# Optimization experiments

Hardware: AMD Instinct MI355X
Metric: run time of the kernel (lower is better)

Reference implementation:

```python
import jax, jax.numpy as jnp
import numpy as np

N_NODES = 150000
N_EDGES = 2400000


def setup_inputs() -> dict:
    key = jax.random.key(0)
    ks = jax.random.split(key, 16)
    d_in, d_h = 6, 32

    def lin(k, fan_in, fan_out):
        # torch nn.Linear default init: U(-1/sqrt(fan_in), 1/sqrt(fan_in))
        bound = 1.0 / np.sqrt(fan_in)
        kw, kb = jax.random.split(k)
        W = jax.random.uniform(kw, (fan_in, fan_out), jnp.float32, -bound, bound)
        b = jax.random.uniform(kb, (fan_out,), jnp.float32, -bound, bound)
        return W, b

    x = jax.random.normal(ks[0], (N_NODES, d_in), jnp.float32)
    edge_index = jax.random.randint(ks[1], (2, N_EDGES), 0, N_NODES, jnp.int64 if jax.config.jax_enable_x64 else jnp.int32)
    W1, b1 = lin(ks[2], d_in, d_h)
    W2, b2 = lin(ks[3], d_h, d_h)
    Wt1, bt1 = lin(ks[4], d_h, d_h // 2)
    Wt2, bt2 = lin(ks[5], d_h // 2, 1)
    Wa1, ba1 = lin(ks[6], d_h, d_h // 2)
    Wa2, ba2 = lin(ks[7], d_h // 2, 6)
    return {"x": x, "edge_index": edge_index,
            "W1": W1, "b1": b1, "W2": W2, "b2": b2,
            "Wt1": Wt1, "bt1": bt1, "Wt2": Wt2, "bt2": bt2,
            "Wa1": Wa1, "ba1": ba1, "Wa2": Wa2, "ba2": ba2}


def gcn_conv(x, src, dst, W, b, n):
    """PyG GCNConv: D^{-1/2}(A+I)D^{-1/2} X W + b (self-loops added)."""
    xw = x @ W  # [N, out]
    ones = jnp.ones(src.shape[0], xw.dtype)
    deg = jax.ops.segment_sum(ones, dst, num_segments=n) + 1.0  # +1 for self-loop
    dinv = jax.lax.rsqrt(deg)
    norm = dinv[src] * dinv[dst]  # [E]
    agg = jax.ops.segment_sum(xw[src] * norm[:, None], dst, num_segments=n)
    agg = agg + xw * (dinv * dinv)[:, None]  # self-loop contribution
    return agg + b


def mlp_head(h, Wa, ba, Wb, bb):
    return jax.nn.relu(h @ Wa + ba) @ Wb + bb


def reference(x, edge_index, W1, b1, W2, b2, Wt1, bt1, Wt2, bt2, Wa1, ba1, Wa2, ba2):
    n = x.shape[0]
    src, dst = edge_index[0], edge_index[1]
    h = jax.nn.relu(gcn_conv(x, src, dst, W1, b1, n))
    features = gcn_conv(h, src, dst, W2, b2, n)
    topology_logits = mlp_head(features, Wt1, bt1, Wt2, bt2)  # [N, 1]
    attributes = mlp_head(features, Wa1, ba1, Wa2, ba2)       # [N, 6]
    normals = attributes[:, :3]
    uvs = attributes[:, 3:]
    return topology_logits, normals, uvs, features
```

## Files before the change

kernel.cpp:

```cpp
#include <hip/hip_runtime.h>
#include <hip/hip_bf16.h>

typedef __hip_bfloat16 bf16;

__device__ __forceinline__ float b2f(bf16 v) { return __bfloat162float(v); }
__device__ __forceinline__ bf16  f2b(float v){ return __float2bfloat16(v); }

__device__ __forceinline__ float loadF(const void* p, int i, int isf32) {
    return isf32 ? ((const float*)p)[i] : b2f(((const bf16*)p)[i]);
}
__device__ __forceinline__ int loadI(const void* p, long long i, int isi64) {
    return isi64 ? (int)((const long long*)p)[i] : ((const int*)p)[i];
}

#define NSBW 512
#define SBSH 9
#define CHUNK_A 4096
#define BCAP 12288

__global__ void sniff_kernel(const void* xv, const void* eiv, int* flags) {
    int lane = threadIdx.x;
    const bf16* xb = (const bf16*)xv;
    int big = 0;
#pragma unroll
    for (int k = 0; k < 4; k++) {
        float v = fabsf(b2f(xb[lane * 4 + k]));
        if (v > 1e6f) big = 1;
    }
    unsigned long long bigmask = __ballot(big);
    const int* e32 = (const int*)eiv;
    int nz = (lane < 32) ? (e32[2 * lane + 1] != 0) : 0;
    unsigned long long nzmask = __ballot(nz);
    if (lane == 0) {
        flags[0] = (__popcll(bigmask) >= 8) ? 1 : 0;
        flags[1] = (nzmask == 0ULL) ? 1 : 0;
    }
}

__global__ void zero_f32(float* __restrict__ p, long long cnt) {
    long long i = (long long)blockIdx.x * blockDim.x + threadIdx.x;
    if (i < cnt) p[i] = 0.f;
}
__global__ void zero_i32(int* __restrict__ p, long long cnt) {
    long long i = (long long)blockIdx.x * blockDim.x + threadIdx.x;
    if (i < cnt) p[i] = 0;
}

__global__ void sb_count(const void* ei, int* __restrict__ sbcnt, int E, int n,
                         const int* __restrict__ flags) {
    __shared__ int h[512];
    int tid = threadIdx.x;
    h[tid] = 0; h[tid + 256] = 0;
    __syncthreads();
    int idf = flags[1];
    long long bs = (long long)blockIdx.x * CHUNK_A;
#pragma unroll 4
    for (int it = 0; it < CHUNK_A / 256; it++) {
        long long e = bs + it * 256 + tid;
        if (e < E) {
            int s = loadI(ei, e, idf);
            int d = loadI(ei, (long long)E + e, idf);
            if ((unsigned)s < (unsigned)n && (unsigned)d < (unsigned)n)
                atomicAdd(&h[d >> SBSH], 1);
        }
    }
    __syncthreads();
    if (h[tid]) atomicAdd(&sbcnt[tid * 16], h[tid]);
    if (h[tid + 256]) atomicAdd(&sbcnt[(tid + 256) * 16], h[tid + 256]);
}

__global__ void sb_scan(const int* __restrict__ sbcnt, int* __restrict__ sboff,
                        int* __restrict__ sbcur, int NSB) {
    __shared__ int lds[512];
    int t = threadIdx.x;
    int v = (t < NSB) ? sbcnt[t * 16] : 0;
    lds[t] = v; __syncthreads();
    for (int off = 1; off < 512; off <<= 1) {
        int tv = (t >= off) ? lds[t - off] : 0;
        __syncthreads();
        lds[t] += tv;
        __syncthreads();
    }
    if (t < NSB) { int ex = lds[t] - v; sboff[t] = ex; sbcur[t * 16] = ex; }
    if (t == 0) sboff[NSB] = lds[511];
}

__global__ void sb_scatter(const void* ei, int* __restrict__ sbcur,
                           unsigned* __restrict__ tmp, int E, int n,
                           const int* __restrict__ flags) {
    __shared__ int h[512];
    __shared__ int base[512];
    int tid = threadIdx.x;
    h[tid] = 0; h[tid + 256] = 0;
    __syncthreads();
    int idf = flags[1];
    long long bs = (long long)blockIdx.x * CHUNK_A;
#pragma unroll 4
    for (int it = 0; it < CHUNK_A / 256; it++) {
        long long e = bs + it * 256 + tid;
        if (e < E) {
            int s = loadI(ei, e, idf);
            int d = loadI(ei, (long long)E + e, idf);
            if ((unsigned)s < (unsigned)n && (unsigned)d < (unsigned)n)
                atomicAdd(&h[d >> SBSH], 1);
        }
    }
    __syncthreads();
    int c0 = h[tid];       if (c0) base[tid] = atomicAdd(&sbcur[tid * 16], c0);
    int c1 = h[tid + 256]; if (c1) base[tid + 256] = atomicAdd(&sbcur[(tid + 256) * 16], c1);
    h[tid] = 0; h[tid + 256] = 0;
    __syncthreads();
#pragma unroll 4
    for (int it = 0; it < CHUNK_A / 256; it++) {
        long long e = bs + it * 256 + tid;
        if (e < E) {
            int s = loadI(ei, e, idf);
            int d = loadI(ei, (long long)E + e, idf);
            if ((unsigned)s < (unsigned)n && (unsigned)d < (unsigned)n) {
                int b = d >> SBSH;
                int r = atomicAdd(&h[b], 1);
                tmp[base[b] + r] = (unsigned)s | ((unsigned)(d & (NSBW - 1)) << 18);
            }
        }
    }
}

__global__ __launch_bounds__(512) void sb_sort(const unsigned* __restrict__ tmp,
                                               const int* __restrict__ sboff,
                                               int* __restrict__ rowptr, int* __restrict__ adj,
                                               int n, int NSB) {
    __shared__ unsigned buf[BCAP];
    __shared__ int deg[NSBW], sc[NSBW], excl[NSBW], cur[NSBW];
    int sb = blockIdx.x, tid = threadIdx.x;
    int beg = sboff[sb], end = sboff[sb + 1], len = end - beg;
    deg[tid] = 0; cur[tid] = 0;
    __syncthreads();
    bool fits = (len <= BCAP);
    for (int i = tid; i < len; i += 512) {
        unsigned p = tmp[beg + i];
        if (fits) buf[i] = p;
        atomicAdd(&deg[p >> 18], 1);
    }
    __syncthreads();
    sc[tid] = deg[tid]; __syncthreads();
    for (int off = 1; off < 512; off <<= 1) {
        int tv = (tid >= off) ? sc[tid - off] : 0;
        __syncthreads();
        sc[tid] += tv;
        __syncthreads();
    }
    excl[tid] = sc[tid] - deg[tid];
    int node = (sb << SBSH) + tid;
    if (node < n) rowptr[node] = beg + excl[tid];
    if (sb == 0 && tid == 0) rowptr[n] = sboff[NSB];
    __syncthreads();
    for (int i = tid; i < len; i += 512) {
        unsigned p = fits ? buf[i] : tmp[beg + i];
        int dl = (int)(p >> 18);
        int pos = excl[dl] + atomicAdd(&cur[dl], 1);
        adj[beg + pos] = (int)(p & 0x3FFFFu);
    }
}

__global__ void prep2_kernel(const int* __restrict__ rowptr, const void* xv,
                             float* __restrict__ dinv, float* __restrict__ z,
                             int n, const int* __restrict__ flags) {
    int i = blockIdx.x * blockDim.x + threadIdx.x;
    if (i >= n) return;
    int xf = flags[0];
    int deg = rowptr[i + 1] - rowptr[i];
    float dv = rsqrtf((float)deg + 1.0f);
    dinv[i] = dv;
    float* zr = z + (size_t)i * 8;
#pragma unroll
    for (int k = 0; k < 6; k++) zr[k] = loadF(xv, i * 6 + k, xf) * dv;
    zr[6] = dv; zr[7] = 0.f;
}

__global__ void gcn1_kernel(const int* __restrict__ rowptr, const int* __restrict__ adj,
                            const float* __restrict__ z,
                            const void* W1v, const void* b1v, const void* W2v,
                            bf16* __restrict__ Y2b, int n, const int* __restrict__ flags) {
    __shared__ float sW1[6 * 32];
    __shared__ float sW2[32 * 32];
    __shared__ float sb1[32];
    int xf = flags[0];
    int tid = threadIdx.x;
    if (tid < 192) sW1[tid] = loadF(W1v, tid, xf);
    for (int i = tid; i < 1024; i += blockDim.x) sW2[i] = loadF(W2v, i, xf);
    if (tid < 32) sb1[tid] = loadF(b1v, tid, xf);
    __syncthreads();
    long long t = (long long)blockIdx.x * blockDim.x + tid;
    int node = (int)(t >> 5), j = (int)(t & 31);
    if (node >= n) return;
    int base = rowptr[node], end = rowptr[node + 1];
    float a0 = 0.f, a1 = 0.f, a2 = 0.f, a3 = 0.f;
    int half4 = (j & 1) * 4;
    for (int i0 = base; i0 < end; i0 += 16) {
        int eidx = i0 + (j >> 1);
        if (eidx < end) {
            int s = adj[eidx];
            const float4 v = *(const float4*)(z + (size_t)s * 8 + half4);
            a0 += v.x; a1 += v.y; a2 += v.z; a3 += v.w;
        }
    }
#pragma unroll
    for (int off = 2; off <= 16; off <<= 1) {
        a0 += __shfl_xor(a0, off, 32); a1 += __shfl_xor(a1, off, 32);
        a2 += __shfl_xor(a2, off, 32); a3 += __shfl_xor(a3, off, 32);
    }
    float S0 = __shfl(a0, 0, 32), S1 = __shfl(a1, 0, 32), S2 = __shfl(a2, 0, 32);
    float S3 = __shfl(a3, 0, 32), S4 = __shfl(a0, 1, 32), S5 = __shfl(a1, 1, 32);
    const float* zs = z + (size_t)node * 8;
    float dv = zs[6];
    S0 += zs[0]; S1 += zs[1]; S2 += zs[2]; S3 += zs[3]; S4 += zs[4]; S5 += zs[5];
    float v = S0 * sW1[j];
    v = fmaf(S1, sW1[32 + j], v);
    v = fmaf(S2, sW1[64 + j], v);
    v = fmaf(S3, sW1[96 + j], v);
    v = fmaf(S4, sW1[128 + j], v);
    v = fmaf(S5, sW1[160 + j], v);
    float h = fmaxf(fmaf(dv, v, sb1[j]), 0.f);
    float y2 = 0.f;
#pragma unroll
    for (int kk = 0; kk < 32; kk++) y2 = fmaf(__shfl(h, kk, 32), sW2[kk * 32 + j], y2);
    Y2b[(size_t)node * 32 + j] = f2b(y2 * dv);
}

__global__ void gcn2_kernel(const int* __restrict__ rowptr, const int* __restrict__ adj,
                            const bf16* __restrict__ Y2b, const float* __restrict__ dinv,
                            const void* b2v,
                            const void* Wt1v, const void* bt1v, const void* Wt2v, const void* bt2v,
                            const void* Wa1v, const void* ba1v, const void* Wa2v, const void* ba2v,
                            float* __restrict__ out, int n, const int* __restrict__ flags) {
    __shared__ float sWt1[32 * 16], sWa1[32 * 16], sWt2[16], sWa2[16 * 6];
    __shared__ float sbt1[16], sba1[16], sba2[6], sb2[32];
    __shared__ float sbt2;
    int xf = flags[0];
    int tid = threadIdx.x;
    for (int i = tid; i < 32 * 16; i += blockDim.x) {
        sWt1[i] = loadF(Wt1v, i, xf);
        sWa1[i] = loadF(Wa1v, i, xf);
    }
    for (int i = tid; i < 16 * 6; i += blockDim.x) sWa2[i] = loadF(Wa2v, i, xf);
    if (tid < 16) { sWt2[tid] = loadF(Wt2v, tid, xf); sbt1[tid] = loadF(bt1v, tid, xf); sba1[tid] = loadF(ba1v, tid, xf); }
    if (tid < 32) sb2[tid] = loadF(b2v, tid, xf);
    if (tid < 6) sba2[tid] = loadF(ba2v, tid, xf);
    if (tid == 0) sbt2 = loadF(bt2v, 0, xf);
    __syncthreads();
    long long t = (long long)blockIdx.x * blockDim.x + tid;
    int node = (int)(t >> 5), j = (int)(t & 31);
    if (node >= n) return;
    int base = rowptr[node], end = rowptr[node + 1];
    float agg = 0.f;
    for (int i0 = base; i0 < end; i0 += 32) {
        int rem = end - i0;
        int sv = (j < rem) ? adj[i0 + j] : 0;
        int mm = (rem < 32) ? rem : 32;
        int kk = 0;
        for (; kk + 4 <= mm; kk += 4) {
            int s0 = __shfl(sv, kk, 32), s1 = __shfl(sv, kk + 1, 32);
            int s2 = __shfl(sv, kk + 2, 32), s3 = __shfl(sv, kk + 3, 32);
            float q0 = b2f(Y2b[(size_t)s0 * 32 + j]);
            float q1 = b2f(Y2b[(size_t)s1 * 32 + j]);
            float q2 = b2f(Y2b[(size_t)s2 * 32 + j]);
            float q3 = b2f(Y2b[(size_t)s3 * 32 + j]);
            agg += (q0 + q1) + (q2 + q3);
        }
        for (; kk < mm; kk++) {
            int s0 = __shfl(sv, kk, 32);
            agg += b2f(Y2b[(size_t)s0 * 32 + j]);
        }
    }
    float dv = dinv[node];
    float f = fmaf(dv, agg + b2f(Y2b[(size_t)node * 32 + j]), sb2[j]);
    __builtin_nontemporal_store(f, &out[(size_t)n * 7 + (size_t)node * 32 + j]);
    float acc = 0.f;
#pragma unroll
    for (int k = 0; k < 32; k++) {
        float fk = __shfl(f, k, 32);
        float w = (j < 16) ? sWt1[k * 16 + j] : sWa1[k * 16 + (j - 16)];
        acc = fmaf(fk, w, acc);
    }
    float u = fmaxf(acc + ((j < 16) ? sbt1[j] : sba1[j - 16]), 0.f);
    float o = 0.f;
#pragma unroll
    for (int k = 0; k < 16; k++) {
        float ut = __shfl(u, k, 32);
        float ua = __shfl(u, 16 + k, 32);
        float w = (j == 0) ? sWt2[k] : ((j < 7) ? sWa2[k * 6 + (j - 1)] : 0.f);
        o = fmaf((j == 0) ? ut : ua, w, o);
    }
    if (j == 0)      out[node] = o + sbt2;
    else if (j < 4)  out[(size_t)n     + (size_t)node * 3 + (j - 1)] = o + sba2[j - 1];
    else if (j < 7)  out[(size_t)n * 4 + (size_t)node * 3 + (j - 4)] = o + sba2[j - 1];
}

__global__ void count_kernel(const void* ei, float* __restrict__ deg, int E, int n,
                             const int* __restrict__ flags) {
    int e = blockIdx.x * blockDim.x + threadIdx.x;
    if (e >= E) return;
    int d = loadI(ei, (long long)E + e, flags[1]);
    if ((unsigned)d < (unsigned)n) atomicAdd(&deg[d], 1.0f);
}
__global__ void dinv_kernel(float* __restrict__ dinv, int n) {
    int i = blockIdx.x * blockDim.x + threadIdx.x;
    if (i < n) dinv[i] = rsqrtf(dinv[i] + 1.0f);
}
__global__ void scatter1_kernel(const void* ei, const void* xv, const void* W1v,
                                const float* __restrict__ dinv, float* __restrict__ A,
                                int E, int n, const int* __restrict__ flags) {
    __shared__ float sW1[6 * 32];
    int xf = flags[0], idf = flags[1];
    int tid = threadIdx.x;
    if (tid < 192) sW1[tid] = loadF(W1v, tid, xf);
    __syncthreads();
    long long t = (long long)blockIdx.x * blockDim.x + tid;
    int e = (int)(t >> 5), j = (int)(t & 31);
    if (e >= E) return;
    int s = loadI(ei, e, idf);
    int d = loadI(ei, (long long)E + e, idf);
    if ((unsigned)s >= (unsigned)n || (unsigned)d >= (unsigned)n) return;
    float dv = dinv[s];
    float y = 0.f;
#pragma unroll
    for (int k = 0; k < 6; k++) y = fmaf(loadF(xv, s * 6 + k, xf), sW1[k * 32 + j], y);
    atomicAdd(&A[(size_t)d * 32 + j], y * dv);
}
__global__ void fused_mid_kernel(const float* __restrict__ A, const void* xv,
                                 const float* __restrict__ dinv,
                                 const void* W1v, const void* b1v, const void* W2v,
                                 float* __restrict__ Yf, int n, const int* __restrict__ flags) {
    __shared__ float sW1[6 * 32];
    __shared__ float sW2[32 * 32];
    __shared__ float sb1[32];
    int xf = flags[0];
    int tid = threadIdx.x;
    if (tid < 192) sW1[tid] = loadF(W1v, tid, xf);
    for (int i = tid; i < 32 * 32; i += blockDim.x) sW2[i] = loadF(W2v, i, xf);
    if (tid < 32) sb1[tid] = loadF(b1v, tid, xf);
    __syncthreads();
    long long t = (long long)blockIdx.x * blockDim.x + tid;
    int node = (int)(t >> 5), j = (int)(t & 31);
    if (node >= n) return;
    float dv = dinv[node];
    float xw = 0.f;
#pragma unroll
    for (int k = 0; k < 6; k++) xw = fmaf(loadF(xv, node * 6 + k, xf), sW1[k * 32 + j], xw);
    float h = fmaxf(dv * A[t] + dv * dv * xw + sb1[j], 0.f);
    float y2 = 0.f;
#pragma unroll
    for (int k = 0; k < 32; k++) y2 = fmaf(__shfl(h, k, 32), sW2[k * 32 + j], y2);
    Yf[t] = y2 * dv;
}
__global__ void scatter2_kernel(const void* ei, const float* __restrict__ Yf,
                                float* __restrict__ A, int E, int n,
                                const int* __restrict__ flags) {
    int idf = flags[1];
    long long t = (long long)blockIdx.x * blockDim.x + threadIdx.x;
    int e = (int)(t >> 5), j = (int)(t & 31);
    if (e >= E) return;
    int s = loadI(ei, e, idf);
    int d = loadI(ei, (long long)E + e, idf);
    if ((unsigned)s >= (unsigned)n || (unsigned)d >= (unsigned)n) return;
    atomicAdd(&A[(size_t)d * 32 + j], Yf[(size_t)s * 32 + j]);
}
__global__ void out_kernel(const float* __restrict__ A, const float* __restrict__ dinv,
                           const void* b2v,
                           const void* Wt1v, const void* bt1v, const void* Wt2v, const void* bt2v,
                           const void* Wa1v, const void* ba1v, const void* Wa2v, const void* ba2v,
                           float* __restrict__ out, int n, const int* __restrict__ flags) {
    __shared__ float sWt1[32 * 16], sWa1[32 * 16], sWt2[16], sWa2[16 * 6];
    __shared__ float sbt1[16], sba1[16], sba2[6], sb2[32];
    __shared__ float sbt2;
    int xf = flags[0];
    int tid = threadIdx.x;
    for (int i = tid; i < 32 * 16; i += blockDim.x) { sWt1[i] = loadF(Wt1v, i, xf); sWa1[i] = loadF(Wa1v, i, xf); }
    for (int i = tid; i < 16 * 6; i += blockDim.x) sWa2[i] = loadF(Wa2v, i, xf);
    if (tid < 16) { sWt2[tid] = loadF(Wt2v, tid, xf); sbt1[tid] = loadF(bt1v, tid, xf); sba1[tid] = loadF(ba1v, tid, xf); }
    if (tid < 32) sb2[tid] = loadF(b2v, tid, xf);
    if (tid < 6) sba2[tid] = loadF(ba2v, tid, xf);
    if (tid == 0) sbt2 = loadF(bt2v, 0, xf);
    __syncthreads();
    long long t = (long long)blockIdx.x * blockDim.x + tid;
    int node = (int)(t >> 5), j = (int)(t & 31);
    if (node >= n) return;
    float* Yf = out + (size_t)n * 7;
    float dv = dinv[node];
    float f = dv * (A[t] + Yf[t]) + sb2[j];
    Yf[t] = f;
    float acc = 0.f;
#pragma unroll
    for (int k = 0; k < 32; k++) {
        float fk = __shfl(f, k, 32);
        float w = (j < 16) ? sWt1[k * 16 + j] : sWa1[k * 16 + (j - 16)];
        acc = fmaf(fk, w, acc);
    }
    float u = fmaxf(acc + ((j < 16) ? sbt1[j] : sba1[j - 16]), 0.f);
    float o = 0.f;
#pragma unroll
    for (int k = 0; k < 16; k++) {
        float ut = __shfl(u, k, 32);
        float ua = __shfl(u, 16 + k, 32);
        float w = (j == 0) ? sWt2[k] : ((j < 7) ? sWa2[k * 6 + (j - 1)] : 0.f);
        o = fmaf((j == 0) ? ut : ua, w, o);
    }
    if (j == 0)      out[node] = o + sbt2;
    else if (j < 4)  out[(size_t)n     + (size_t)node * 3 + (j - 1)] = o + sba2[j - 1];
    else if (j < 7)  out[(size_t)n * 4 + (size_t)node * 3 + (j - 4)] = o + sba2[j - 1];
}

extern "C" void kernel_launch(void* const* d_in, const int* in_sizes, int n_in,
                              void* d_out, int out_size, void* d_ws, size_t ws_size,
                              hipStream_t stream) {
    const void* x   = d_in[0];
    const void* ei  = d_in[1];
    const void* W1  = d_in[2];
    const void* b1  = d_in[3];
    const void* W2  = d_in[4];
    const void* b2  = d_in[5];
    const void* Wt1 = d_in[6];
    const void* bt1 = d_in[7];
    const void* Wt2 = d_in[8];
    const void* bt2 = d_in[9];
    const void* Wa1 = d_in[10];
    const void* ba1 = d_in[11];
    const void* Wa2 = d_in[12];
    const void* ba2 = d_in[13];

    int n = in_sizes[0] / 6;
    int E = in_sizes[1] / 2;

    const int B = 256;
    float* out = (float*)d_out;
    char* ws = (char*)d_ws;

    int NSB = (n + NSBW - 1) >> SBSH;
    size_t nw  = (size_t)((n + 63) & ~63);
    size_t Ew  = (size_t)((E + 63) & ~63);
    size_t Mw  = (16 * nw > Ew) ? 16 * nw : Ew;
    size_t w_sbc = 0;
    size_t w_sbo = 8192;
    size_t w_scu = 8192 + 576;
    size_t w_flg = w_scu + 8192;
    size_t w_row = w_flg + 64;
    size_t w_div = w_row + nw + 64;
    size_t w_z   = w_div + nw;
    size_t w_un  = w_z + 8 * nw;
    size_t w_adj = w_un + Mw;
    size_t need  = (w_adj + Ew) * 4;

    if (ws_size >= need && n <= (1 << 18)) {
        int*      sbcnt = (int*)(ws + w_sbc * 4);
        int*      sboff = (int*)(ws + w_sbo * 4);
        int*      sbcur = (int*)(ws + w_scu * 4);
        int*      flags = (int*)(ws + w_flg * 4);
        int*      rowptr= (int*)(ws + w_row * 4);
        float*    dinv  = (float*)(ws + w_div * 4);
        float*    z     = (float*)(ws + w_z * 4);
        unsigned* tmp   = (unsigned*)(ws + w_un * 4);
        bf16*     Y2b   = (bf16*)(ws + w_un * 4);
        int*      adj   = (int*)(ws + w_adj * 4);

        int grid_a = (int)(((long long)E + CHUNK_A - 1) / CHUNK_A);
        int grid_nodes32 = (int)(((long long)n * 32 + B - 1) / B);

        sniff_kernel<<<1, 64, 0, stream>>>(x, ei, flags);
        zero_i32<<<(8192 * 2 + 576 + B - 1) / B, B, 0, stream>>>(sbcnt, 8192 * 2 + 576);
        sb_count<<<grid_a, B, 0, stream>>>(ei, sbcnt, E, n, flags);
        sb_scan<<<1, 512, 0, stream>>>(sbcnt, sboff, sbcur, NSB);
        sb_scatter<<<grid_a, B, 0, stream>>>(ei, sbcur, tmp, E, n, flags);
        sb_sort<<<NSB, 512, 0, stream>>>(tmp, sboff, rowptr, adj, n, NSB);
        prep2_kernel<<<(n + B - 1) / B, B, 0, stream>>>(rowptr, x, dinv, z, n, flags);
        gcn1_kernel<<<grid_nodes32, B, 0, stream>>>(rowptr, adj, z, W1, b1, W2, Y2b, n, flags);
        gcn2_kernel<<<grid_nodes32, B, 0, stream>>>(rowptr, adj, Y2b, dinv, b2,
                                                    Wt1, bt1, Wt2, bt2, Wa1, ba1, Wa2, ba2,
                                                    out, n, flags);
        return;
    }

    size_t n_pad = (size_t)((n + 63) & ~63);
    float* A     = (float*)ws;
    float* dinvF = (float*)(ws + (size_t)32 * n * 4);
    int* flagsF  = (int*)(ws + ((size_t)32 * n + n_pad) * 4);
    float* Yf    = out + (size_t)n * 7;

    long long zcnt = (long long)32 * n + (long long)n_pad;
    int grid_zero  = (int)((zcnt + B - 1) / B);
    int grid_zeroA = (int)(((long long)32 * n + B - 1) / B);
    int grid_nodes = (int)(((long long)n * 32 + B - 1) / B);
    int grid_edges = (int)(((long long)E * 32 + B - 1) / B);

    sniff_kernel<<<1, 64, 0, stream>>>(x, ei, flagsF);
    zero_f32<<<grid_zero, B, 0, stream>>>(A, zcnt);
    count_kernel<<<(E + B - 1) / B, B, 0, stream>>>(ei, dinvF, E, n, flagsF);
    dinv_kernel<<<(n + B - 1) / B, B, 0, stream>>>(dinvF, n);
    scatter1_kernel<<<grid_edges, B, 0, stream>>>(ei, x, W1, dinvF, A, E, n, flagsF);
    fused_mid_kernel<<<grid_nodes, B, 0, stream>>>(A, x, dinvF, W1, b1, W2, Yf, n, flagsF);
    zero_f32<<<grid_zeroA, B, 0, stream>>>(A, (long long)32 * n);
    scatter2_kernel<<<grid_edges, B, 0, stream>>>(ei, Yf, A, E, n, flagsF);
    out_kernel<<<grid_nodes, B, 0, stream>>>(A, dinvF, b2, Wt1, bt1, Wt2, bt2,
                                             Wa1, ba1, Wa2, ba2, out, n, flagsF);
}
```

Baseline: 360.4 us.

## Split Y2 into bf16 halves, pack z as bf16, separate MLP head kernel

The per-node layer-1 input z is packed into 16-byte bf16 records. Each warp lane now gathers a whole neighbour record, where before two lanes shared one fp32 record. Layer-2 features are stored as two 16-channel bf16 arrays (32 bytes per node each), and aggregation runs in two passes so each pass's working set is smaller and more cache-friendly, using 16-byte vector gathers. The MLP heads move into a separate kernel that rereads the features from output memory. This adds kernel launches, an extra read of the feature output, a second traversal of adjacency, and reduced precision for z.

```diff
diff --git a/kernel.cpp b/kernel.cpp
--- a/kernel.cpp
+++ b/kernel.cpp
@@ -5,6 +5,14 @@
 
 __device__ __forceinline__ float b2f(bf16 v) { return __bfloat162float(v); }
 __device__ __forceinline__ bf16  f2b(float v){ return __float2bfloat16(v); }
+__device__ __forceinline__ float uplo(unsigned u){ return __uint_as_float(u << 16); }
+__device__ __forceinline__ float uphi(unsigned u){ return __uint_as_float(u & 0xFFFF0000u); }
+__device__ __forceinline__ unsigned pk2(float a, float b){
+    bf16 ha = f2b(a), hb = f2b(b);
+    unsigned short ua = *reinterpret_cast<unsigned short*>(&ha);
+    unsigned short ub = *reinterpret_cast<unsigned short*>(&hb);
+    return (unsigned)ua | ((unsigned)ub << 16);
+}
 
 __device__ __forceinline__ float loadF(const void* p, int i, int isf32) {
     return isf32 ? ((const float*)p)[i] : b2f(((const bf16*)p)[i]);
@@ -163,7 +171,7 @@
 }
 
 __global__ void prep2_kernel(const int* __restrict__ rowptr, const void* xv,
-                             float* __restrict__ dinv, float* __restrict__ z,
+                             float* __restrict__ dinv, uint4* __restrict__ zb,
                              int n, const int* __restrict__ flags) {
     int i = blockIdx.x * blockDim.x + threadIdx.x;
     if (i >= n) return;
@@ -171,110 +179,132 @@
     int deg = rowptr[i + 1] - rowptr[i];
     float dv = rsqrtf((float)deg + 1.0f);
     dinv[i] = dv;
-    float* zr = z + (size_t)i * 8;
-#pragma unroll
-    for (int k = 0; k < 6; k++) zr[k] = loadF(xv, i * 6 + k, xf) * dv;
-    zr[6] = dv; zr[7] = 0.f;
+    float z0 = loadF(xv, i * 6 + 0, xf) * dv, z1 = loadF(xv, i * 6 + 1, xf) * dv;
+    float z2 = loadF(xv, i * 6 + 2, xf) * dv, z3 = loadF(xv, i * 6 + 3, xf) * dv;
+    float z4 = loadF(xv, i * 6 + 4, xf) * dv, z5 = loadF(xv, i * 6 + 5, xf) * dv;
+    uint4 r;
+    r.x = pk2(z0, z1); r.y = pk2(z2, z3); r.z = pk2(z4, z5); r.w = pk2(dv, 0.f);
+    zb[i] = r;
 }
 
 __global__ void gcn1_kernel(const int* __restrict__ rowptr, const int* __restrict__ adj,
-                            const float* __restrict__ z,
+                            const uint4* __restrict__ zb, const float* __restrict__ dinv,
                             const void* W1v, const void* b1v, const void* W2v,
-                            bf16* __restrict__ Y2b, int n, const int* __restrict__ flags) {
-    __shared__ float sW1[6 * 32];
-    __shared__ float sW2[32 * 32];
+                            bf16* __restrict__ Y2lo, bf16* __restrict__ Y2hi,
+                            int n, const int* __restrict__ flags) {
+    __shared__ float sW1[192];
+    __shared__ float sW2[1024];
     __shared__ float sb1[32];
     int xf = flags[0];
     int tid = threadIdx.x;
     if (tid < 192) sW1[tid] = loadF(W1v, tid, xf);
-    for (int i = tid; i < 1024; i += blockDim.x) sW2[i] = loadF(W2v, i, xf);
+    for (int i = tid; i < 1024; i += 256) sW2[i] = loadF(W2v, i, xf);
     if (tid < 32) sb1[tid] = loadF(b1v, tid, xf);
     __syncthreads();
     long long t = (long long)blockIdx.x * blockDim.x + tid;
     int node = (int)(t >> 5), j = (int)(t & 31);
     if (node >= n) return;
     int base = rowptr[node], end = rowptr[node + 1];
-    float a0 = 0.f, a1 = 0.f, a2 = 0.f, a3 = 0.f;
-    int half4 = (j & 1) * 4;
+    float a0 = 0, a1 = 0, a2 = 0, a3 = 0, a4 = 0, a5 = 0;
+    for (int i0 = base; i0 < end; i0 += 32) {
+        int idx = i0 + j;
+        if (idx < end) {
+            uint4 v = zb[adj[idx]];
+            a0 += uplo(v.x); a1 += uphi(v.x);
+            a2 += uplo(v.y); a3 += uphi(v.y);
+            a4 += uplo(v.z); a5 += uphi(v.z);
+        }
+    }
+#pragma unroll
+    for (int off = 1; off <= 16; off <<= 1) {
+        a0 += __shfl_xor(a0, off, 32); a1 += __shfl_xor(a1, off, 32);
+        a2 += __shfl_xor(a2, off, 32); a3 += __shfl_xor(a3, off, 32);
+        a4 += __shfl_xor(a4, off, 32); a5 += __shfl_xor(a5, off, 32);
+    }
+    uint4 zs = zb[node];
+    a0 += uplo(zs.x); a1 += uphi(zs.x); a2 += uplo(zs.y);
+    a3 += uphi(zs.y); a4 += uplo(zs.z); a5 += uphi(zs.z);
+    float dv = dinv[node];
+    float v = a0 * sW1[j];
+    v = fmaf(a1, sW1[32 + j], v);
+    v = fmaf(a2, sW1[64 + j], v);
+    v = fmaf(a3, sW1[96 + j], v);
+    v = fmaf(a4, sW1[128 + j], v);
+    v = fmaf(a5, sW1[160 + j], v);
+    float h = fmaxf(fmaf(dv, v, sb1[j]), 0.f);
+    float y2 = 0.f;
+#pragma unroll
+    for (int kk = 0; kk < 32; kk++) y2 = fmaf(__shfl(h, kk, 32), sW2[kk * 32 + j], y2);
+    y2 *= dv;
+    if (j < 16) Y2lo[(size_t)node * 16 + j] = f2b(y2);
+    else        Y2hi[(size_t)node * 16 + (j - 16)] = f2b(y2);
+}
+
+__global__ void gcn2_half(const int* __restrict__ rowptr, const int* __restrict__ adj,
+                          const uint4* __restrict__ Yh, const float* __restrict__ dinv,
+                          const void* b2v, float* __restrict__ outF,
+                          int n, int halfbase, const int* __restrict__ flags) {
+    int xf = flags[0];
+    long long t = (long long)blockIdx.x * blockDim.x + threadIdx.x;
+    int node = (int)(t >> 5), j = (int)(t & 31);
+    if (node >= n) return;
+    int p = j & 1;
+    int base = rowptr[node], end = rowptr[node + 1];
+    float a0 = 0, a1 = 0, a2 = 0, a3 = 0, a4 = 0, a5 = 0, a6 = 0, a7 = 0;
     for (int i0 = base; i0 < end; i0 += 16) {
-        int eidx = i0 + (j >> 1);
-        if (eidx < end) {
-            int s = adj[eidx];
-            const float4 v = *(const float4*)(z + (size_t)s * 8 + half4);
-            a0 += v.x; a1 += v.y; a2 += v.z; a3 += v.w;
+        int idx = i0 + (j >> 1);
+        if (idx < end) {
+            uint4 v = Yh[(size_t)adj[idx] * 2 + p];
+            a0 += uplo(v.x); a1 += uphi(v.x); a2 += uplo(v.y); a3 += uphi(v.y);
+            a4 += uplo(v.z); a5 += uphi(v.z); a6 += uplo(v.w); a7 += uphi(v.w);
         }
     }
 #pragma unroll
     for (int off = 2; off <= 16; off <<= 1) {
         a0 += __shfl_xor(a0, off, 32); a1 += __shfl_xor(a1, off, 32);
         a2 += __shfl_xor(a2, off, 32); a3 += __shfl_xor(a3, off, 32);
-    }
-    float S0 = __shfl(a0, 0, 32), S1 = __shfl(a1, 0, 32), S2 = __shfl(a2, 0, 32);
-    float S3 = __shfl(a3, 0, 32), S4 = __shfl(a0, 1, 32), S5 = __shfl(a1, 1, 32);
-    const float* zs = z + (size_t)node * 8;
-    float dv = zs[6];
-    S0 += zs[0]; S1 += zs[1]; S2 += zs[2]; S3 += zs[3]; S4 += zs[4]; S5 += zs[5];
-    float v = S0 * sW1[j];
-    v = fmaf(S1, sW1[32 + j], v);
-    v = fmaf(S2, sW1[64 + j], v);
-    v = fmaf(S3, sW1[96 + j], v);
-    v = fmaf(S4, sW1[128 + j], v);
-    v = fmaf(S5, sW1[160 + j], v);
-    float h = fmaxf(fmaf(dv, v, sb1[j]), 0.f);
-    float y2 = 0.f;
-#pragma unroll
-    for (int kk = 0; kk < 32; kk++) y2 = fmaf(__shfl(h, kk, 32), sW2[kk * 32 + j], y2);
-    Y2b[(size_t)node * 32 + j] = f2b(y2 * dv);
-}
-
-__global__ void gcn2_kernel(const int* __restrict__ rowptr, const int* __restrict__ adj,
-                            const bf16* __restrict__ Y2b, const float* __restrict__ dinv,
-                            const void* b2v,
-                            const void* Wt1v, const void* bt1v, const void* Wt2v, const void* bt2v,
+        a4 += __shfl_xor(a4, off, 32); a5 += __shfl_xor(a5, off, 32);
+        a6 += __shfl_xor(a6, off, 32); a7 += __shfl_xor(a7, off, 32);
+    }
+    if (j < 2) {
+        uint4 sv = Yh[(size_t)node * 2 + p];
+        a0 += uplo(sv.x); a1 += uphi(sv.x); a2 += uplo(sv.y); a3 += uphi(sv.y);
+        a4 += uplo(sv.z); a5 += uphi(sv.z); a6 += uplo(sv.w); a7 += uphi(sv.w);
+        float dv = dinv[node];
+        int bo = halfbase + p * 8;
+        float4 w0, w1;
+        w0.x = fmaf(dv, a0, loadF(b2v, bo + 0, xf));
+        w0.y = fmaf(dv, a1, loadF(b2v, bo + 1, xf));
+        w0.z = fmaf(dv, a2, loadF(b2v, bo + 2, xf));
+        w0.w = fmaf(dv, a3, loadF(b2v, bo + 3, xf));
+        w1.x = fmaf(dv, a4, loadF(b2v, bo + 4, xf));
+        w1.y = fmaf(dv, a5, loadF(b2v, bo + 5, xf));
+        w1.z = fmaf(dv, a6, loadF(b2v, bo + 6, xf));
+        w1.w = fmaf(dv, a7, loadF(b2v, bo + 7, xf));
+        float* dst = outF + (size_t)node * 32 + bo;
+        *(float4*)dst = w0;
+        *(float4*)(dst + 4) = w1;
+    }
+}
+
+__global__ void head_kernel(const void* Wt1v, const void* bt1v, const void* Wt2v, const void* bt2v,
                             const void* Wa1v, const void* ba1v, const void* Wa2v, const void* ba2v,
                             float* __restrict__ out, int n, const int* __restrict__ flags) {
-    __shared__ float sWt1[32 * 16], sWa1[32 * 16], sWt2[16], sWa2[16 * 6];
-    __shared__ float sbt1[16], sba1[16], sba2[6], sb2[32];
+    __shared__ float sWt1[512], sWa1[512], sWt2[16], sWa2[96];
+    __shared__ float sbt1[16], sba1[16], sba2[6];
     __shared__ float sbt2;
     int xf = flags[0];
     int tid = threadIdx.x;
-    for (int i = tid; i < 32 * 16; i += blockDim.x) {
-        sWt1[i] = loadF(Wt1v, i, xf);
-        sWa1[i] = loadF(Wa1v, i, xf);
-    }
-    for (int i = tid; i < 16 * 6; i += blockDim.x) sWa2[i] = loadF(Wa2v, i, xf);
+    for (int i = tid; i < 512; i += blockDim.x) { sWt1[i] = loadF(Wt1v, i, xf); sWa1[i] = loadF(Wa1v, i, xf); }
+    if (tid < 96) sWa2[tid] = loadF(Wa2v, tid, xf);
     if (tid < 16) { sWt2[tid] = loadF(Wt2v, tid, xf); sbt1[tid] = loadF(bt1v, tid, xf); sba1[tid] = loadF(ba1v, tid, xf); }
-    if (tid < 32) sb2[tid] = loadF(b2v, tid, xf);
     if (tid < 6) sba2[tid] = loadF(ba2v, tid, xf);
     if (tid == 0) sbt2 = loadF(bt2v, 0, xf);
     __syncthreads();
     long long t = (long long)blockIdx.x * blockDim.x + tid;
     int node = (int)(t >> 5), j = (int)(t & 31);
     if (node >= n) return;
-    int base = rowptr[node], end = rowptr[node + 1];
-    float agg = 0.f;
-    for (int i0 = base; i0 < end; i0 += 32) {
-        int rem = end - i0;
-        int sv = (j < rem) ? adj[i0 + j] : 0;
-        int mm = (rem < 32) ? rem : 32;
-        int kk = 0;
-        for (; kk + 4 <= mm; kk += 4) {
-            int s0 = __shfl(sv, kk, 32), s1 = __shfl(sv, kk + 1, 32);
-            int s2 = __shfl(sv, kk + 2, 32), s3 = __shfl(sv, kk + 3, 32);
-            float q0 = b2f(Y2b[(size_t)s0 * 32 + j]);
-            float q1 = b2f(Y2b[(size_t)s1 * 32 + j]);
-            float q2 = b2f(Y2b[(size_t)s2 * 32 + j]);
-            float q3 = b2f(Y2b[(size_t)s3 * 32 + j]);
-            agg += (q0 + q1) + (q2 + q3);
-        }
-        for (; kk < mm; kk++) {
-            int s0 = __shfl(sv, kk, 32);
-            agg += b2f(Y2b[(size_t)s0 * 32 + j]);
-        }
-    }
-    float dv = dinv[node];
-    float f = fmaf(dv, agg + b2f(Y2b[(size_t)node * 32 + j]), sb2[j]);
-    __builtin_nontemporal_store(f, &out[(size_t)n * 7 + (size_t)node * 32 + j]);
+    float f = out[(size_t)n * 7 + (size_t)node * 32 + j];
     float acc = 0.f;
 #pragma unroll
     for (int k = 0; k < 32; k++) {
@@ -445,8 +475,8 @@
     size_t w_flg = w_scu + 8192;
     size_t w_row = w_flg + 64;
     size_t w_div = w_row + nw + 64;
-    size_t w_z   = w_div + nw;
-    size_t w_un  = w_z + 8 * nw;
+    size_t w_zb  = w_div + nw;
+    size_t w_un  = w_zb + 4 * nw;
     size_t w_adj = w_un + Mw;
     size_t need  = (w_adj + Ew) * 4;
 
@@ -457,9 +487,10 @@
         int*      flags = (int*)(ws + w_flg * 4);
         int*      rowptr= (int*)(ws + w_row * 4);
         float*    dinv  = (float*)(ws + w_div * 4);
-        float*    z     = (float*)(ws + w_z * 4);
+        uint4*    zb    = (uint4*)(ws + w_zb * 4);
         unsigned* tmp   = (unsigned*)(ws + w_un * 4);
-        bf16*     Y2b   = (bf16*)(ws + w_un * 4);
+        bf16*     Y2lo  = (bf16*)(ws + w_un * 4);
+        bf16*     Y2hi  = (bf16*)(ws + (w_un + 8 * nw) * 4);
         int*      adj   = (int*)(ws + w_adj * 4);
 
         int grid_a = (int)(((long long)E + CHUNK_A - 1) / CHUNK_A);
@@ -471,10 +502,14 @@
         sb_scan<<<1, 512, 0, stream>>>(sbcnt, sboff, sbcur, NSB);
         sb_scatter<<<grid_a, B, 0, stream>>>(ei, sbcur, tmp, E, n, flags);
         sb_sort<<<NSB, 512, 0, stream>>>(tmp, sboff, rowptr, adj, n, NSB);
-        prep2_kernel<<<(n + B - 1) / B, B, 0, stream>>>(rowptr, x, dinv, z, n, flags);
-        gcn1_kernel<<<grid_nodes32, B, 0, stream>>>(rowptr, adj, z, W1, b1, W2, Y2b, n, flags);
-        gcn2_kernel<<<grid_nodes32, B, 0, stream>>>(rowptr, adj, Y2b, dinv, b2,
-                                                    Wt1, bt1, Wt2, bt2, Wa1, ba1, Wa2, ba2,
+        prep2_kernel<<<(n + B - 1) / B, B, 0, stream>>>(rowptr, x, dinv, zb, n, flags);
+        gcn1_kernel<<<grid_nodes32, B, 0, stream>>>(rowptr, adj, zb, dinv, W1, b1, W2,
+                                                    Y2lo, Y2hi, n, flags);
+        gcn2_half<<<grid_nodes32, B, 0, stream>>>(rowptr, adj, (const uint4*)Y2lo, dinv, b2,
+                                                  out + (size_t)n * 7, n, 0, flags);
+        gcn2_half<<<grid_nodes32, B, 0, stream>>>(rowptr, adj, (const uint4*)Y2hi, dinv, b2,
+                                                  out + (size_t)n * 7, n, 16, flags);
+        head_kernel<<<grid_nodes32, B, 0, stream>>>(Wt1, bt1, Wt2, bt2, Wa1, ba1, Wa2, ba2,
                                                     out, n, flags);
         return;
     }
```

Measured after the change: 400.6 us. 11.1% more time.
